# Performance work log

Measured on AMD Instinct MI355X. Metric: run time of the kernel, lower is better.

Reference implementation:

```python
import jax, jax.numpy as jnp
import numpy as np

EPS = 1e-5

def layer_norm(x, w, b):
    mu = x.mean(-1, keepdims=True)
    var = x.var(-1, keepdims=True)
    return (x - mu) / jnp.sqrt(var + EPS) * w + b

def moe_ffn(y, gW, W1, b1, W2, b2, topk):
    # y: [B,N,d]; W1: [E,d,f]; W2: [E,f,d].  Dense-equivalent of the
    # torch gather/compute/scatter-add dispatch: every expert runs on every
    # token, combined with top-k gate weights (zero for unselected experts).
    gate = jax.nn.softmax(y @ gW, axis=-1)                       # [B,N,E]
    w, sel = jax.lax.top_k(gate, topk)                           # [B,N,k]
    onehot = jax.nn.one_hot(sel, gW.shape[-1], dtype=y.dtype)    # [B,N,k,E]
    comb = jnp.einsum('bnk,bnke->bne', w, onehot)                # combine weights
    hmid = jax.nn.gelu(jnp.einsum('bnd,edf->bnef', y, W1) + b1, approximate=False)
    eo = jnp.einsum('bnef,efd->bned', hmid, W2) + b2             # [B,N,E,d]
    out = jnp.einsum('bne,bned->bnd', comb, eo)
    mask = onehot.sum(2)                                         # [B,N,E] 0/1
    cnt = mask.sum((0, 1))                                       # tokens per expert
    emb = jnp.einsum('bne,bnd->ed', mask, y) / jnp.maximum(cnt, 1.0)[:, None]
    return out, gate, emb

def setup_inputs():
    B, S, N = 8, 512, 1024
    d, H, E, f, L, topk = 512, 8, 8, 8, 2, 2   # d_ff == n_heads (repo quirk)
    key = jax.random.key(0)
    ks = iter(jax.random.split(key, 40))
    g = lambda shape, s=0.02: jax.random.normal(next(ks), shape, jnp.float32) * s
    return dict(
        x=jax.random.normal(next(ks), (B, S, N), jnp.float32),
        revin_w=jnp.ones((N,), jnp.float32) + g((N,), 0.01),
        revin_b=g((N,), 0.01),
        emb_W=g((S, d)), emb_b=g((d,)),
        Wq=g((L, d, d)), bq=g((L, d)),
        Wk=g((L, d, d)), bk=g((L, d)),
        Wv=g((L, d, d)), bv=g((L, d)),
        Wo=g((L, d, d)), bo=g((L, d)),
        ln1_w=jnp.ones((L, d), jnp.float32), ln1_b=jnp.zeros((L, d), jnp.float32),
        ln2_w=jnp.ones((L, d), jnp.float32), ln2_b=jnp.zeros((L, d), jnp.float32),
        gate_W=g((L, d, E)),
        eW1=g((L, E, d, f)), eb1=g((L, E, f)),
        eW2=g((L, E, f, d)), eb2=g((L, E, d)),
        enc_norm_w=jnp.ones((d,), jnp.float32), enc_norm_b=jnp.zeros((d,), jnp.float32),
        head_gate_W=g((d, E)),
        head_W=g((E, d, d)), head_b=g((E, d)),
        topk=topk, n_heads=H,
    )

def reference(x, revin_w, revin_b, emb_W, emb_b, Wq, bq, Wk, bk, Wv, bv, Wo, bo,
              ln1_w, ln1_b, ln2_w, ln2_b, gate_W, eW1, eb1, eW2, eb2,
              enc_norm_w, enc_norm_b, head_gate_W, head_W, head_b, topk, n_heads):
    B, S, N = x.shape
    d = emb_W.shape[1]
    H = n_heads
    dh = d // H
    L = Wq.shape[0]
    # RevIN normalize over time per variable (dropout layers are eval/identity)
    xv = jnp.swapaxes(x, 1, 2)                                   # [B,N,S]
    mean = xv.mean(-1, keepdims=True)
    std = jnp.sqrt(xv.var(-1, keepdims=True) + EPS)
    xn = (xv - mean) / std * revin_w[None, :, None] + revin_b[None, :, None]
    # DataEmbedding_inverted: Linear over the time axis -> variable tokens
    h = xn @ emb_W + emb_b                                       # [B,N,d]
    for l in range(L):
        q = (h @ Wq[l] + bq[l]).reshape(B, N, H, dh)
        k = (h @ Wk[l] + bk[l]).reshape(B, N, H, dh)
        v = (h @ Wv[l] + bv[l]).reshape(B, N, H, dh)
        attn = jax.nn.softmax(jnp.einsum('bnhe,bmhe->bhnm', q, k) / jnp.sqrt(jnp.float32(dh)), axis=-1)
        o = jnp.einsum('bhnm,bmhe->bnhe', attn, v).reshape(B, N, d) @ Wo[l] + bo[l]
        h = layer_norm(h + o, ln1_w[l], ln1_b[l])
        ffn, _gate, _emb = moe_ffn(h, gate_W[l], eW1[l], eb1[l], eW2[l], eb2[l], topk)
        h = layer_norm(h + ffn, ln2_w[l], ln2_b[l])
    h = layer_norm(h, enc_norm_w, enc_norm_b)
    # MoE projection head: experts are Linear(d, d)
    gate = jax.nn.softmax(h @ head_gate_W, axis=-1)
    w, sel = jax.lax.top_k(gate, topk)
    onehot = jax.nn.one_hot(sel, head_gate_W.shape[-1], dtype=h.dtype)
    comb = jnp.einsum('bnk,bnke->bne', w, onehot)
    eo = jnp.einsum('bnd,edf->bnef', h, head_W) + head_b         # [B,N,E,d]
    out = jnp.einsum('bne,bned->bnd', comb, eo)                  # [B,N,d]
    # RevIN denorm applied on [B, d_model, N]
    o2 = jnp.swapaxes(out, 1, 2)
    o2 = (o2 - revin_b[None, None, :]) / (revin_w[None, None, :] + 1e-10)
    o2 = o2 * jnp.swapaxes(std, 1, 2) + jnp.swapaxes(mean, 1, 2)
    return jnp.swapaxes(o2, 1, 2)                                # [B, n_vars, d_model]
```

## Files before the change

kernel.cpp:

```cpp
#include <hip/hip_runtime.h>
#include <math.h>

#define BATCH 8
#define SEQ 512
#define NVAR 1024
#define DM 512
#define NH 8
#define DH 64
#define NE 8
#define NF 8
#define NL 2
#define NTOK (BATCH*NVAR)
#define LN_EPS 1e-5f
#define LSC 2048.0f
#define ILSC (1.0f/2048.0f)

typedef __attribute__((ext_vector_type(8))) _Float16 f16x8;
typedef __attribute__((ext_vector_type(2))) _Float16 f16x2;
typedef __attribute__((ext_vector_type(4))) float f32x4;
#define MFMA16 __builtin_amdgcn_mfma_f32_16x16x32_f16

__device__ __forceinline__ void fsplit(float v, _Float16& hi, _Float16& lo) {
    hi = (_Float16)v;
    lo = (_Float16)((v - (float)hi) * LSC);
}
__device__ __forceinline__ float frec(_Float16 hi, _Float16 lo) {
    return (float)hi + (float)lo * ILSC;
}
__device__ __forceinline__ void fsplit2(float a, float b, f16x2& h2, f16x2& l2) {
    h2 = __builtin_bit_cast(f16x2, __builtin_amdgcn_cvt_pkrtz(a, b));
    l2 = __builtin_bit_cast(f16x2, __builtin_amdgcn_cvt_pkrtz(
             (a - (float)h2.x)*LSC, (b - (float)h2.y)*LSC));
}

__device__ __forceinline__ void gload_lds16(const _Float16* g, _Float16* l) {
    __builtin_amdgcn_global_load_lds(
        (const __attribute__((address_space(1))) void*)g,
        (__attribute__((address_space(3))) void*)l, 16, 0, 0);
}

#define DPPROR(v, C) __int_as_float(__builtin_amdgcn_update_dpp(0, __float_as_int(v), (C), 0xF, 0xF, true))
__device__ __forceinline__ float rowmax16(float v) {
    v = fmaxf(v, DPPROR(v, 0x121));
    v = fmaxf(v, DPPROR(v, 0x122));
    v = fmaxf(v, DPPROR(v, 0x124));
    v = fmaxf(v, DPPROR(v, 0x128));
    return v;
}
__device__ __forceinline__ float rowsum16(float v) {
    v += DPPROR(v, 0x121);
    v += DPPROR(v, 0x122);
    v += DPPROR(v, 0x124);
    v += DPPROR(v, 0x128);
    return v;
}

__global__ __launch_bounds__(256) void revin_stats_kernel(
        const float* __restrict__ x, float* __restrict__ mean, float* __restrict__ stdd) {
    int blk = blockIdx.x;
    int b = blk >> 4;
    int n0 = (blk & 15) << 6;
    int t = threadIdx.x;
    int ni = t & 63, sg = t >> 6;
    float s = 0.f, ss = 0.f;
    for (int sidx = sg; sidx < SEQ; sidx += 4) {
        float v = x[((size_t)b*SEQ + sidx)*NVAR + n0 + ni];
        s += v; ss += v*v;
    }
    __shared__ float rs[4][64], rq[4][64];
    rs[sg][ni] = s; rq[sg][ni] = ss;
    __syncthreads();
    if (t < 64) {
        float su = rs[0][t] + rs[1][t] + rs[2][t] + rs[3][t];
        float sq = rq[0][t] + rq[1][t] + rq[2][t] + rq[3][t];
        float m  = su / (float)SEQ;
        float var = sq / (float)SEQ - m*m;
        int n = n0 + t;
        mean[b*NVAR + n] = m;
        stdd[b*NVAR + n] = sqrtf(var + LN_EPS);
    }
}

__global__ __launch_bounds__(256) void revin_norm_kernel(
        const float* __restrict__ x, const float* __restrict__ mean, const float* __restrict__ stdd,
        const float* __restrict__ rw, const float* __restrict__ rb,
        _Float16* __restrict__ xnhi, _Float16* __restrict__ xnlo) {
    __shared__ float tile[32][33];
    int n0 = blockIdx.x << 5, s0 = blockIdx.y << 5, b = blockIdx.z;
    int t = threadIdx.x;
    int j = t & 31, i0 = t >> 5;
    for (int ii = i0; ii < 32; ii += 8)
        tile[ii][j] = x[((size_t)b*SEQ + s0 + ii)*NVAR + n0 + j];
    __syncthreads();
    int si = t & 31, j0 = t >> 5;
    for (int nj = j0; nj < 32; nj += 8) {
        int n = n0 + nj;
        float m = mean[b*NVAR + n], sd = stdd[b*NVAR + n];
        float v = (tile[si][nj] - m) / sd * rw[n] + rb[n];
        _Float16 h_, l_; fsplit(v, h_, l_);
        size_t idx = ((size_t)b*NVAR + n)*SEQ + s0 + si;
        xnhi[idx] = h_; xnlo[idx] = l_;
    }
}

struct WSrcs { const float* p[9]; };
__global__ __launch_bounds__(256) void transpose_w_kernel(
        WSrcs srcs, _Float16* __restrict__ whi, _Float16* __restrict__ wlo) {
    const float* W = srcs.p[blockIdx.z];
    _Float16* oh = whi + (size_t)blockIdx.z * DM * DM;
    _Float16* ol = wlo + (size_t)blockIdx.z * DM * DM;
    __shared__ float tile[64][65];
    int k0 = blockIdx.x << 6, n0 = blockIdx.y << 6;
    int t = threadIdx.x;
    for (int idx = t; idx < 4096; idx += 256) {
        int k = idx >> 6, n = idx & 63;
        tile[k][n] = W[(size_t)(k0 + k)*DM + n0 + n];
    }
    __syncthreads();
    for (int idx = t; idx < 4096; idx += 256) {
        int n = idx >> 6, k = idx & 63;
        _Float16 h_, l_; fsplit(tile[k][n], h_, l_);
        size_t o = (size_t)(n0 + n)*DM + k0 + k;
        oh[o] = h_; ol[o] = l_;
    }
}

__global__ __launch_bounds__(256) void gemm_f16x2_kernel(
        const _Float16* __restrict__ Ahg, const _Float16* __restrict__ Alg,
        const _Float16* __restrict__ Whg, const _Float16* __restrict__ Wlg,
        const float* __restrict__ bias, float* __restrict__ C,
        _Float16* __restrict__ Chi, _Float16* __restrict__ Clo,
        int M, int K, int N) {
    __shared__ _Float16 smem[24576];
    int id = blockIdx.x + (blockIdx.y << 3);
    int rm = ((id & 7) << 6) | (id >> 3);
    int bm = (rm >> 3) << 7, bn = (rm & 7) << 6;
    int t = threadIdx.x;
    int w = t >> 6, lane = t & 63, m16 = lane & 15, quad = lane >> 4;
    int wv = __builtin_amdgcn_readfirstlane(w);
    int lrow = lane >> 2, lcol = (lane & 3) << 3;
    f32x4 a1[2][4] = {}, a2[2][4] = {};

    #define G_STAGE(c, kk) do {                                              \
        _Pragma("unroll")                                                    \
        for (int ch = 0; ch < 2; ++ch) {                                     \
            size_t ga = (size_t)(bm + wv*32 + ch*16 + lrow)*K + (kk) + lcol; \
            gload_lds16(&Ahg[ga], &smem[(c)*4096 + (wv*32 + ch*16)*32]);     \
            gload_lds16(&Alg[ga], &smem[8192 + (c)*4096 + (wv*32 + ch*16)*32]); \
        }                                                                    \
        size_t gb = (size_t)(bn + wv*16 + lrow)*K + (kk) + lcol;             \
        gload_lds16(&Whg[gb], &smem[16384 + (c)*2048 + (wv*16)*32]);         \
        gload_lds16(&Wlg[gb], &smem[20480 + (c)*2048 + (wv*16)*32]);         \
    } while (0)

    G_STAGE(0, 0);
    int cur = 0;
    for (int k0 = 0; k0 < K; k0 += 32, cur ^= 1) {
        __syncthreads();
        if (k0 + 32 < K) G_STAGE(cur ^ 1, k0 + 32);
        const _Float16* AH = &smem[cur*4096];
        const _Float16* AL = &smem[8192 + cur*4096];
        const _Float16* BH = &smem[16384 + cur*2048];
        const _Float16* BL = &smem[20480 + cur*2048];
        f16x8 bh_[4], bl_[4];
#pragma unroll
        for (int nt = 0; nt < 4; ++nt) {
            bh_[nt] = *(const f16x8*)&BH[(nt*16 + m16)*32 + quad*8];
            bl_[nt] = *(const f16x8*)&BL[(nt*16 + m16)*32 + quad*8];
        }
#pragma unroll
        for (int h2 = 0; h2 < 2; ++h2) {
            f16x8 ah = *(const f16x8*)&AH[(w*32 + h2*16 + m16)*32 + quad*8];
            f16x8 al = *(const f16x8*)&AL[(w*32 + h2*16 + m16)*32 + quad*8];
#pragma unroll
            for (int nt = 0; nt < 4; ++nt) {
                a1[h2][nt] = MFMA16(ah, bh_[nt], a1[h2][nt], 0, 0, 0);
                a2[h2][nt] = MFMA16(ah, bl_[nt], a2[h2][nt], 0, 0, 0);
                a2[h2][nt] = MFMA16(al, bh_[nt], a2[h2][nt], 0, 0, 0);
            }
        }
    }
    #undef G_STAGE
#pragma unroll
    for (int h2 = 0; h2 < 2; ++h2)
#pragma unroll
        for (int nt = 0; nt < 4; ++nt) {
            int col = bn + nt*16 + m16;
            float bv = bias[col];
#pragma unroll
            for (int r = 0; r < 4; ++r) {
                size_t row = bm + w*32 + h2*16 + quad*4 + r;
                float v = a1[h2][nt][r] + a2[h2][nt][r]*ILSC + bv;
                if (C) C[row*N + col] = v;
                if (Chi) {
                    _Float16 h_, l_; fsplit(v, h_, l_);
                    Chi[row*N + col] = h_; Clo[row*N + col] = l_;
                }
            }
        }
}

__global__ __launch_bounds__(256) void gemm_qkvt_kernel(
        const _Float16* __restrict__ Ahg, const _Float16* __restrict__ Alg,
        const _Float16* __restrict__ Wqkh, const _Float16* __restrict__ Wqkl,
        const _Float16* __restrict__ Wvh,  const _Float16* __restrict__ Wvl,
        const float* __restrict__ biasQ, const float* __restrict__ biasK,
        const float* __restrict__ biasV,
        _Float16* __restrict__ Qhi, _Float16* __restrict__ Qlo,
        _Float16* __restrict__ KKhi, _Float16* __restrict__ KKlo,
        _Float16* __restrict__ vthi, _Float16* __restrict__ vtlo) {
    __shared__ _Float16 smem[24576];
    int t = threadIdx.x;
    int w = t >> 6, lane = t & 63, m16 = lane & 15, quad = lane >> 4;
    int wv = __builtin_amdgcn_readfirstlane(w);
    int lrow = lane >> 2, lcol = (lane & 3) << 3;

    if (blockIdx.x < 1024) {
        int id = blockIdx.x;
        int rm = ((id & 7) << 7) | (id >> 3);
        int bm = (rm >> 4) << 7, bn = (rm & 15) << 6;
        f32x4 a1[2][4] = {}, a2[2][4] = {};
        #define QK_STAGE(c, kk) do {                                             \
            _Pragma("unroll")                                                    \
            for (int ch = 0; ch < 2; ++ch) {                                     \
                size_t ga = (size_t)(bm + wv*32 + ch*16 + lrow)*DM + (kk) + lcol;\
                gload_lds16(&Ahg[ga], &smem[(c)*4096 + (wv*32 + ch*16)*32]);     \
                gload_lds16(&Alg[ga], &smem[8192 + (c)*4096 + (wv*32 + ch*16)*32]); \
            }                                                                    \
            size_t gb = (size_t)(bn + wv*16 + lrow)*DM + (kk) + lcol;            \
            gload_lds16(&Wqkh[gb], &smem[16384 + (c)*2048 + (wv*16)*32]);        \
            gload_lds16(&Wqkl[gb], &smem[20480 + (c)*2048 + (wv*16)*32]);        \
        } while (0)
        QK_STAGE(0, 0);
        int cur = 0;
        for (int k0 = 0; k0 < DM; k0 += 32, cur ^= 1) {
            __syncthreads();
            if (k0 + 32 < DM) QK_STAGE(cur ^ 1, k0 + 32);
            const _Float16* AH = &smem[cur*4096];
            const _Float16* AL = &smem[8192 + cur*4096];
            const _Float16* BH = &smem[16384 + cur*2048];
            const _Float16* BL = &smem[20480 + cur*2048];
            f16x8 bh_[4], bl_[4];
#pragma unroll
            for (int nt = 0; nt < 4; ++nt) {
                bh_[nt] = *(const f16x8*)&BH[(nt*16 + m16)*32 + quad*8];
                bl_[nt] = *(const f16x8*)&BL[(nt*16 + m16)*32 + quad*8];
            }
#pragma unroll
            for (int h2 = 0; h2 < 2; ++h2) {
                f16x8 ah = *(const f16x8*)&AH[(w*32 + h2*16 + m16)*32 + quad*8];
                f16x8 al = *(const f16x8*)&AL[(w*32 + h2*16 + m16)*32 + quad*8];
#pragma unroll
                for (int nt = 0; nt < 4; ++nt) {
                    a1[h2][nt] = MFMA16(ah, bh_[nt], a1[h2][nt], 0, 0, 0);
                    a2[h2][nt] = MFMA16(ah, bl_[nt], a2[h2][nt], 0, 0, 0);
                    a2[h2][nt] = MFMA16(al, bh_[nt], a2[h2][nt], 0, 0, 0);
                }
            }
        }
        #undef QK_STAGE
        const float* bias = (bn < 512) ? biasQ : biasK;
        _Float16* Ohi = (bn < 512) ? Qhi : KKhi;
        _Float16* Olo = (bn < 512) ? Qlo : KKlo;
        int cb = (bn < 512) ? bn : bn - 512;
#pragma unroll
        for (int h2 = 0; h2 < 2; ++h2)
#pragma unroll
            for (int nt = 0; nt < 4; ++nt) {
                int col = cb + nt*16 + m16;
                float bv = bias[col];
#pragma unroll
                for (int r = 0; r < 4; ++r) {
                    size_t row = bm + w*32 + h2*16 + quad*4 + r;
                    float v = a1[h2][nt][r] + a2[h2][nt][r]*ILSC + bv;
                    _Float16 h_, l_; fsplit(v, h_, l_);
                    Ohi[row*DM + col] = h_; Olo[row*DM + col] = l_;
                }
            }
        return;
    }
    {
        int id = blockIdx.x - 1024;
        int rm = ((id & 7) << 6) | (id >> 3);
        int bm = (rm >> 3) << 7, bn = (rm & 7) << 6;
        f32x4 a1[2][4] = {}, a2[2][4] = {};
        #define VT_STAGE(c, kk) do {                                             \
            _Pragma("unroll")                                                    \
            for (int ch = 0; ch < 2; ++ch) {                                     \
                size_t ga = (size_t)(bm + wv*32 + ch*16 + lrow)*DM + (kk) + lcol;\
                gload_lds16(&Ahg[ga], &smem[(c)*4096 + (wv*32 + ch*16)*32]);     \
                gload_lds16(&Alg[ga], &smem[8192 + (c)*4096 + (wv*32 + ch*16)*32]); \
            }                                                                    \
            size_t gb = (size_t)(bn + wv*16 + lrow)*DM + (kk) + lcol;            \
            gload_lds16(&Wvh[gb], &smem[16384 + (c)*2048 + (wv*16)*32]);         \
            gload_lds16(&Wvl[gb], &smem[20480 + (c)*2048 + (wv*16)*32]);         \
        } while (0)
        VT_STAGE(0, 0);
        int cur = 0;
        for (int k0 = 0; k0 < DM; k0 += 32, cur ^= 1) {
            __syncthreads();
            if (k0 + 32 < DM) VT_STAGE(cur ^ 1, k0 + 32);
            const _Float16* AH = &smem[cur*4096];
            const _Float16* AL = &smem[8192 + cur*4096];
            const _Float16* BH = &smem[16384 + cur*2048];
            const _Float16* BL = &smem[20480 + cur*2048];
            f16x8 bh_[4], bl_[4];
#pragma unroll
            for (int nt = 0; nt < 4; ++nt) {
                bh_[nt] = *(const f16x8*)&BH[(nt*16 + m16)*32 + quad*8];
                bl_[nt] = *(const f16x8*)&BL[(nt*16 + m16)*32 + quad*8];
            }
#pragma unroll
            for (int h2 = 0; h2 < 2; ++h2) {
                f16x8 ah = *(const f16x8*)&AH[(w*32 + h2*16 + m16)*32 + quad*8];
                f16x8 al = *(const f16x8*)&AL[(w*32 + h2*16 + m16)*32 + quad*8];
#pragma unroll
                for (int nt = 0; nt < 4; ++nt) {
                    a1[h2][nt] = MFMA16(ah, bh_[nt], a1[h2][nt], 0, 0, 0);
                    a2[h2][nt] = MFMA16(ah, bl_[nt], a2[h2][nt], 0, 0, 0);
                    a2[h2][nt] = MFMA16(al, bh_[nt], a2[h2][nt], 0, 0, 0);
                }
            }
        }
        #undef VT_STAGE
        __syncthreads();
        float (*Ct)[65] = (float (*)[65])smem;
#pragma unroll
        for (int h2 = 0; h2 < 2; ++h2)
#pragma unroll
            for (int nt = 0; nt < 4; ++nt) {
                float bv = biasV[bn + nt*16 + m16];
#pragma unroll
                for (int r = 0; r < 4; ++r)
                    Ct[w*32 + h2*16 + quad*4 + r][nt*16 + m16] = a1[h2][nt][r] + a2[h2][nt][r]*ILSC + bv;
            }
        __syncthreads();
        int b = bm >> 10, tokn0 = bm & 1023, hh = bn >> 6;
        int dh = t >> 2, tg = (t & 3) << 4;
        size_t rowb = ((size_t)(b*8 + hh)*64 + dh)*NVAR + tokn0;
        for (int hb = 0; hb < 2; ++hb) {
            int tl0 = hb*64 + tg;
            unsigned short hbuf[16], lbuf[16];
#pragma unroll
            for (int i = 0; i < 16; ++i) {
                _Float16 h_, l_; fsplit(Ct[tl0 + i][dh], h_, l_);
                hbuf[i] = __builtin_bit_cast(unsigned short, h_);
                lbuf[i] = __builtin_bit_cast(unsigned short, l_);
            }
            uint4 uh0, uh1, ul0, ul1;
            uh0.x = hbuf[0]|(hbuf[1]<<16);  uh0.y = hbuf[2]|(hbuf[3]<<16);
            uh0.z = hbuf[4]|(hbuf[5]<<16);  uh0.w = hbuf[6]|(hbuf[7]<<16);
            uh1.x = hbuf[8]|(hbuf[9]<<16);  uh1.y = hbuf[10]|(hbuf[11]<<16);
            uh1.z = hbuf[12]|(hbuf[13]<<16);uh1.w = hbuf[14]|(hbuf[15]<<16);
            ul0.x = lbuf[0]|(lbuf[1]<<16);  ul0.y = lbuf[2]|(lbuf[3]<<16);
            ul0.z = lbuf[4]|(lbuf[5]<<16);  ul0.w = lbuf[6]|(lbuf[7]<<16);
            ul1.x = lbuf[8]|(lbuf[9]<<16);  ul1.y = lbuf[10]|(lbuf[11]<<16);
            ul1.z = lbuf[12]|(lbuf[13]<<16);ul1.w = lbuf[14]|(lbuf[15]<<16);
            *(uint4*)&vthi[rowb + tl0]     = uh0;
            *(uint4*)&vthi[rowb + tl0 + 8] = uh1;
            *(uint4*)&vtlo[rowb + tl0]     = ul0;
            *(uint4*)&vtlo[rowb + tl0 + 8] = ul1;
        }
    }
}

__global__ __launch_bounds__(256, 4) void attn_f16x2_kernel(
        const _Float16* __restrict__ qh, const _Float16* __restrict__ ql,
        const _Float16* __restrict__ kh, const _Float16* __restrict__ kl,
        const _Float16* __restrict__ vth, const _Float16* __restrict__ vtl,
        _Float16* __restrict__ oh, _Float16* __restrict__ ol) {
    __shared__ _Float16 Kh[64][72], Kl[64][72];
    __shared__ _Float16 Vh[64][72], Vl[64][72];
    int blk = blockIdx.x;
    blk = ((blk & 7) << 7) | (blk >> 3);
    int qt = blk & 15, bh = blk >> 4;
    int b = bh >> 3, hh = bh & 7;
    int q0 = qt << 6;
    int t = threadIdx.x;
    int w = t >> 6, lane = t & 63;
    int m16 = lane & 15, quad = lane >> 4;
    size_t bbase = (size_t)b * NVAR;
    size_t vbase = (size_t)bh * DH * NVAR;

    f16x8 qfh[2], qfl[2];
#pragma unroll
    for (int ks = 0; ks < 2; ++ks) {
        size_t gq = (bbase + q0 + w*16 + m16)*DM + hh*DH + ks*32 + quad*8;
        qfh[ks] = *(const f16x8*)&qh[gq] * (_Float16)0.125f;
        qfl[ks] = *(const f16x8*)&ql[gq] * (_Float16)0.125f;
    }

    float mrow[4] = {-1e30f,-1e30f,-1e30f,-1e30f};
    float lrow[4] = {0.f,0.f,0.f,0.f};
    f32x4 o1[4] = {}, o2[4] = {};

    for (int n0 = 0; n0 < NVAR; n0 += 64) {
        for (int idx = t; idx < 512; idx += 256) {
            int r = idx >> 3, cg = (idx & 7) << 3;
            size_t gk = (bbase + n0 + r)*DM + hh*DH + cg;
            size_t gv = vbase + (size_t)r*NVAR + n0 + cg;
            *(uint4*)&Kh[r][cg] = *(const uint4*)&kh[gk];
            *(uint4*)&Kl[r][cg] = *(const uint4*)&kl[gk];
            *(uint4*)&Vh[r][cg] = *(const uint4*)&vth[gv];
            *(uint4*)&Vl[r][cg] = *(const uint4*)&vtl[gv];
        }
        __syncthreads();

        f32x4 s1[4] = {}, s2[4] = {};
#pragma unroll
        for (int ks = 0; ks < 2; ++ks) {
#pragma unroll
            for (int nt = 0; nt < 4; ++nt) {
                f16x8 bh_ = *(const f16x8*)&Kh[nt*16 + m16][ks*32 + quad*8];
                f16x8 bl_ = *(const f16x8*)&Kl[nt*16 + m16][ks*32 + quad*8];
                s1[nt] = MFMA16(qfh[ks], bh_, s1[nt], 0, 0, 0);
                s2[nt] = MFMA16(qfh[ks], bl_, s2[nt], 0, 0, 0);
                s2[nt] = MFMA16(qfl[ks], bh_, s2[nt], 0, 0, 0);
            }
        }
        __syncthreads();

        float pbuf[4][4];
        float mx[4];
#pragma unroll
        for (int r = 0; r < 4; ++r) {
            float sv0 = fmaf(s2[0][r], ILSC, s1[0][r]);
            float sv1 = fmaf(s2[1][r], ILSC, s1[1][r]);
            float sv2 = fmaf(s2[2][r], ILSC, s1[2][r]);
            float sv3 = fmaf(s2[3][r], ILSC, s1[3][r]);
            pbuf[0][r] = sv0; pbuf[1][r] = sv1; pbuf[2][r] = sv2; pbuf[3][r] = sv3;
            mx[r] = rowmax16(fmaxf(fmaxf(sv0, sv1), fmaxf(sv2, sv3)));
        }
        bool grow = (mx[0] > mrow[0]) | (mx[1] > mrow[1]) |
                    (mx[2] > mrow[2]) | (mx[3] > mrow[3]);
        if (__any(grow)) {
#pragma unroll
            for (int r = 0; r < 4; ++r) {
                float mnew = fmaxf(mrow[r], mx[r]);
                float alpha = __expf(mrow[r] - mnew);
                mrow[r] = mnew;
                lrow[r] *= alpha;
#pragma unroll
                for (int nt = 0; nt < 4; ++nt) { o1[nt][r] *= alpha; o2[nt][r] *= alpha; }
            }
        }
#pragma unroll
        for (int r = 0; r < 4; ++r) {
            float p0 = __expf(pbuf[0][r] - mrow[r]);
            float p1 = __expf(pbuf[1][r] - mrow[r]);
            float p2 = __expf(pbuf[2][r] - mrow[r]);
            float p3 = __expf(pbuf[3][r] - mrow[r]);
            lrow[r] += rowsum16(p0 + p1 + p2 + p3);
            pbuf[0][r] = p0; pbuf[1][r] = p1; pbuf[2][r] = p2; pbuf[3][r] = p3;
        }
#pragma unroll
        for (int nt = 0; nt < 4; ++nt)
#pragma unroll
            for (int rp = 0; rp < 2; ++rp) {
                f16x2 h2, l2;
                fsplit2(pbuf[nt][2*rp], pbuf[nt][2*rp + 1], h2, l2);
                Kh[w*16 + quad*4 + 2*rp][nt*16 + m16]     = h2.x;
                Kh[w*16 + quad*4 + 2*rp + 1][nt*16 + m16] = h2.y;
                Kl[w*16 + quad*4 + 2*rp][nt*16 + m16]     = l2.x;
                Kl[w*16 + quad*4 + 2*rp + 1][nt*16 + m16] = l2.y;
            }

#pragma unroll
        for (int ks = 0; ks < 2; ++ks) {
            f16x8 ph = *(const f16x8*)&Kh[w*16 + m16][ks*32 + quad*8];
            f16x8 pl = *(const f16x8*)&Kl[w*16 + m16][ks*32 + quad*8];
#pragma unroll
            for (int nt = 0; nt < 4; ++nt) {
                f16x8 vh_ = *(const f16x8*)&Vh[nt*16 + m16][ks*32 + quad*8];
                f16x8 vl_ = *(const f16x8*)&Vl[nt*16 + m16][ks*32 + quad*8];
                o1[nt] = MFMA16(ph, vh_, o1[nt], 0, 0, 0);
                o2[nt] = MFMA16(ph, vl_, o2[nt], 0, 0, 0);
                o2[nt] = MFMA16(pl, vh_, o2[nt], 0, 0, 0);
            }
        }
        __syncthreads();
    }
#pragma unroll
    for (int r = 0; r < 4; ++r) {
        float inv = 1.0f / lrow[r];
        size_t rowp = (bbase + q0 + w*16 + quad*4 + r)*DM + hh*DH;
        float ovv[4];
#pragma unroll
        for (int nt = 0; nt < 4; ++nt)
            ovv[nt] = fmaf(o2[nt][r], ILSC, o1[nt][r]) * inv;
#pragma unroll
        for (int np = 0; np < 2; ++np) {
            f16x2 h2, l2;
            fsplit2(ovv[2*np], ovv[2*np + 1], h2, l2);
            oh[rowp + (2*np)*16 + m16]     = h2.x;
            oh[rowp + (2*np + 1)*16 + m16] = h2.y;
            ol[rowp + (2*np)*16 + m16]     = l2.x;
            ol[rowp + (2*np + 1)*16 + m16] = l2.y;
        }
    }
}

__global__ __launch_bounds__(256) void ln_kernel(
        _Float16* __restrict__ hhi, _Float16* __restrict__ hlo,
        const float* __restrict__ res,
        const float* __restrict__ w, const float* __restrict__ b) {
    int rowi = blockIdx.x, t = threadIdx.x;
    size_t base = (size_t)rowi * DM;
    int c = t << 1;
    f16x2 hv = *(const f16x2*)&hhi[base + c];
    f16x2 lv = *(const f16x2*)&hlo[base + c];
    float v0 = frec(hv.x, lv.x);
    float v1 = frec(hv.y, lv.y);
    if (res) { float2 rv = *(const float2*)&res[base + c]; v0 += rv.x; v1 += rv.y; }
    float s = v0 + v1, q = v0*v0 + v1*v1;
#pragma unroll
    for (int off = 1; off < 64; off <<= 1) {
        s += __shfl_xor(s, off);
        q += __shfl_xor(q, off);
    }
    __shared__ float sred[4], qred[4];
    int wid = t >> 6, lane = t & 63;
    if (lane == 0) { sred[wid] = s; qred[wid] = q; }
    __syncthreads();
    s = sred[0] + sred[1] + sred[2] + sred[3];
    q = qred[0] + qred[1] + qred[2] + qred[3];
    float m = s / (float)DM;
    float var = q / (float)DM - m*m;
    float inv = 1.0f / sqrtf(var + LN_EPS);
    float2 wv = *(const float2*)&w[c];
    float2 bv = *(const float2*)&b[c];
    float y0 = (v0 - m)*inv * wv.x + bv.x;
    float y1 = (v1 - m)*inv * wv.y + bv.y;
    f16x2 h2, l2; fsplit2(y0, y1, h2, l2);
    *(f16x2*)&hhi[base + c] = h2;
    *(f16x2*)&hlo[base + c] = l2;
}

__device__ __forceinline__ float gelu_exact(float xv) {
    return 0.5f * xv * (1.0f + erff(xv * 0.70710678118654752f));
}

__global__ __launch_bounds__(256) void moe_ln_kernel(
        _Float16* __restrict__ hhi, _Float16* __restrict__ hlo,
        const float* __restrict__ gW, const float* __restrict__ W1, const float* __restrict__ b1,
        const float* __restrict__ W2, const float* __restrict__ b2,
        const float* __restrict__ lw, const float* __restrict__ lb) {
    int tok = blockIdx.x, t = threadIdx.x;
    __shared__ float hs[DM];
    __shared__ float red[32][8];
    __shared__ float glog[8];
    __shared__ float hmid[8];
    __shared__ float wsel[2];
    __shared__ int   esel[2];
    __shared__ float sred[4], qred[4];
    size_t base = (size_t)tok * DM;
    int c = t << 1;
    f16x2 hv = *(const f16x2*)&hhi[base + c];
    f16x2 lv = *(const f16x2*)&hlo[base + c];
    float hv0 = frec(hv.x, lv.x);
    float hv1 = frec(hv.y, lv.y);
    hs[c] = hv0; hs[c + 1] = hv1;
    __syncthreads();
    int e = t & 7, i0 = t >> 3;
    {
        float a = 0.f;
        for (int i = i0; i < DM; i += 32) a += hs[i] * gW[i*NE + e];
        red[i0][e] = a;
    }
    __syncthreads();
    if (t < 8) { float sv = 0.f; for (int i = 0; i < 32; ++i) sv += red[i][t]; glog[t] = sv; }
    __syncthreads();
    if (t == 0) {
        float m0 = -1e30f, m1 = -1e30f; int s0i = 0, s1i = 0;
        for (int ei = 0; ei < 8; ++ei) {
            float vv = glog[ei];
            if (vv > m0) { m1 = m0; s1i = s0i; m0 = vv; s0i = ei; }
            else if (vv > m1) { m1 = vv; s1i = ei; }
        }
        float Z = 0.f;
        for (int ei = 0; ei < 8; ++ei) Z += expf(glog[ei] - m0);
        wsel[0] = 1.0f / Z;
        wsel[1] = expf(m1 - m0) / Z;
        esel[0] = s0i; esel[1] = s1i;
    }
    __syncthreads();
    float o0 = 0.f, o1 = 0.f;
    for (int ks = 0; ks < 2; ++ks) {
        int ee = esel[ks]; float wk = wsel[ks];
        int f = t & 7;
        float a = 0.f;
        for (int i = i0; i < DM; i += 32) a += hs[i] * W1[((size_t)ee*DM + i)*NF + f];
        red[i0][f] = a;
        __syncthreads();
        if (t < 8) {
            float sv = b1[ee*NF + t];
            for (int i = 0; i < 32; ++i) sv += red[i][t];
            hmid[t] = gelu_exact(sv);
        }
        __syncthreads();
        float2 b2v = *(const float2*)&b2[ee*DM + c];
        float s0v = b2v.x, s1v = b2v.y;
#pragma unroll
        for (int i = 0; i < NF; ++i) {
            float hm = hmid[i];
            float2 wpv = *(const float2*)&W2[((size_t)ee*NF + i)*DM + c];
            s0v += hm * wpv.x; s1v += hm * wpv.y;
        }
        o0 += wk * s0v; o1 += wk * s1v;
        __syncthreads();
    }
    float v0 = hv0 + o0, v1 = hv1 + o1;
    float s = v0 + v1, q = v0*v0 + v1*v1;
#pragma unroll
    for (int off = 1; off < 64; off <<= 1) {
        s += __shfl_xor(s, off);
        q += __shfl_xor(q, off);
    }
    int wid = t >> 6, lane = t & 63;
    if (lane == 0) { sred[wid] = s; qred[wid] = q; }
    __syncthreads();
    s = sred[0] + sred[1] + sred[2] + sred[3];
    q = qred[0] + qred[1] + qred[2] + qred[3];
    float m = s / (float)DM;
    float var = q / (float)DM - m*m;
    float inv = 1.0f / sqrtf(var + LN_EPS);
    float2 wv = *(const float2*)&lw[c];
    float2 bv = *(const float2*)&lb[c];
    float y0 = (v0 - m)*inv * wv.x + bv.x;
    float y1 = (v1 - m)*inv * wv.y + bv.y;
    f16x2 h2o, l2o; fsplit2(y0, y1, h2o, l2o);
    *(f16x2*)&hhi[base + c] = h2o;
    *(f16x2*)&hlo[base + c] = l2o;
}

__global__ __launch_bounds__(256) void encln_gate_kernel(
        _Float16* __restrict__ hhi, _Float16* __restrict__ hlo,
        const float* __restrict__ lw, const float* __restrict__ lb,
        const float* __restrict__ gW,
        int* __restrict__ sel, float2* __restrict__ wpair,
        int* __restrict__ cnt) {
    int tok = blockIdx.x, t = threadIdx.x;
    if (tok == 0 && t < NE) cnt[t] = 0;
    __shared__ float hs[DM];
    __shared__ float red[32][8];
    __shared__ float glog[8];
    __shared__ float sred[4], qred[4];
    size_t base = (size_t)tok * DM;
    int c = t << 1;
    f16x2 hv = *(const f16x2*)&hhi[base + c];
    f16x2 lv = *(const f16x2*)&hlo[base + c];
    float v0 = frec(hv.x, lv.x);
    float v1 = frec(hv.y, lv.y);
    float s = v0 + v1, q = v0*v0 + v1*v1;
#pragma unroll
    for (int off = 1; off < 64; off <<= 1) {
        s += __shfl_xor(s, off);
        q += __shfl_xor(q, off);
    }
    int wid = t >> 6, lane = t & 63;
    if (lane == 0) { sred[wid] = s; qred[wid] = q; }
    __syncthreads();
    s = sred[0] + sred[1] + sred[2] + sred[3];
    q = qred[0] + qred[1] + qred[2] + qred[3];
    float m = s / (float)DM;
    float var = q / (float)DM - m*m;
    float inv = 1.0f / sqrtf(var + LN_EPS);
    float2 wv = *(const float2*)&lw[c];
    float2 bv = *(const float2*)&lb[c];
    float y0 = (v0 - m)*inv * wv.x + bv.x;
    float y1 = (v1 - m)*inv * wv.y + bv.y;
    f16x2 h2o, l2o; fsplit2(y0, y1, h2o, l2o);
    *(f16x2*)&hhi[base + c] = h2o;
    *(f16x2*)&hlo[base + c] = l2o;
    hs[c] = y0; hs[c + 1] = y1;
    __syncthreads();
    int e = t & 7, i0 = t >> 3;
    float a = 0.f;
    for (int i = i0; i < DM; i += 32) a += hs[i] * gW[i*NE + e];
    red[i0][e] = a;
    __syncthreads();
    if (t < 8) { float sv = 0.f; for (int i = 0; i < 32; ++i) sv += red[i][t]; glog[t] = sv; }
    __syncthreads();
    if (t == 0) {
        float m0 = -1e30f, m1 = -1e30f; int s0i = 0, s1i = 0;
        for (int ei = 0; ei < 8; ++ei) {
            float vv = glog[ei];
            if (vv > m0) { m1 = m0; s1i = s0i; m0 = vv; s0i = ei; }
            else if (vv > m1) { m1 = vv; s1i = ei; }
        }
        float Z = 0.f;
        for (int ei = 0; ei < 8; ++ei) Z += __expf(glog[ei] - m0);
        float2 wvv;
        wvv.x = 1.0f / Z;
        wvv.y = __expf(m1 - m0) / Z;
        sel[tok] = s0i | (s1i << 3);
        wpair[tok] = wvv;
    }
}

__global__ __launch_bounds__(64) void head_bucket_kernel(
        const int* __restrict__ sel, const float2* __restrict__ wpair,
        int* __restrict__ cnt, int* __restrict__ idxlist, float* __restrict__ wlist,
        int* __restrict__ pos0, int* __restrict__ pos1) {
    int lane = threadIdx.x;
    int tok = blockIdx.x*64 + lane;
    int s = sel[tok];
    int s0 = s & 7, s1 = (s >> 3) & 7;
    float2 wv = wpair[tok];
    unsigned long long lmask = (lane == 63) ? 0x7FFFFFFFFFFFFFFFull
                                            : ((1ull << lane) - 1ull);
#pragma unroll
    for (int e = 0; e < NE; ++e) {
        unsigned long long m0 = __ballot(s0 == e);
        unsigned long long m1 = __ballot(s1 == e);
        int tot = __popcll(m0) + __popcll(m1);
        int basep = 0;
        if (lane == 0 && tot > 0) basep = atomicAdd(&cnt[e], tot);
        basep = __shfl(basep, 0);
        if (s0 == e) {
            int p = basep + __popcll(m0 & lmask);
            idxlist[e*NTOK + p] = tok; wlist[e*NTOK + p] = wv.x;
            pos0[tok] = (e << 16) | p;
        }
        if (s1 == e) {
            int p = basep + __popcll(m0) + __popcll(m1 & lmask);
            idxlist[e*NTOK + p] = tok; wlist[e*NTOK + p] = wv.y;
            pos1[tok] = (e << 16) | p;
        }
    }
}

__global__ __launch_bounds__(64) void head_prefix_kernel(int* __restrict__ cnt) {
    if (threadIdx.x == 0) {
        int run = 0, trun = 0;
        for (int e = 0; e < NE; ++e) {
            cnt[8 + e]  = run;  run  += cnt[e];
            cnt[16 + e] = trun; trun += (cnt[e] + 63) >> 6;
        }
        cnt[24] = trun;
    }
}

__global__ __launch_bounds__(256) void head_gemm_f16x2_kernel(
        const _Float16* __restrict__ hhi, const _Float16* __restrict__ hlo,
        const _Float16* __restrict__ hwhi, const _Float16* __restrict__ hwlo,
        const float* __restrict__ Hb,
        const int* __restrict__ cnt, const int* __restrict__ idxlist,
        const float* __restrict__ wlist, float* __restrict__ slotf) {
    int item = blockIdx.x;
    int total = cnt[24];
    if (item >= 2*total) return;
    int bn   = (item & 1) << 8;
    int tile = item >> 1;
    int e = 0;
#pragma unroll
    for (int ei = 1; ei < NE; ++ei) if (tile >= cnt[16 + ei]) e = ei;
    int m0 = (tile - cnt[16 + e]) << 6;
    int cnt_e = cnt[e];
    int rv = cnt_e - m0; if (rv > 64) rv = 64;
    int pref_e = cnt[8 + e];
    int t = threadIdx.x;
    int w = t >> 6, lane = t & 63, m16 = lane & 15, quad = lane >> 4;

    __shared__ _Float16 sAh[64][40], sAl[64][40];
    __shared__ _Float16 sBh[256][40], sBl[256][40];
    __shared__ int   idxs[64];
    __shared__ float ws[64];
    if (t < 64) {
        if (t < rv) { idxs[t] = idxlist[e*NTOK + m0 + t]; ws[t] = wlist[e*NTOK + m0 + t]; }
        else        { idxs[t] = idxlist[e*NTOK + m0];     ws[t] = 0.f; }
    }
    __syncthreads();

    const _Float16* Wh = hwhi + (size_t)e*DM*DM;
    const _Float16* Wl = hwlo + (size_t)e*DM*DM;
    int ra = t >> 2, ca = (t & 3) << 3;
    f32x4 a1[4][4] = {}, a2[4][4] = {};
    for (int k0 = 0; k0 < DM; k0 += 32) {
        size_t ga = (size_t)idxs[ra]*DM + k0 + ca;
        *(uint4*)&sAh[ra][ca] = *(const uint4*)&hhi[ga];
        *(uint4*)&sAl[ra][ca] = *(const uint4*)&hlo[ga];
#pragma unroll
        for (int p = 0; p < 4; ++p) {
            int rb = p*64 + ra;
            size_t gb = (size_t)(bn + rb)*DM + k0 + ca;
            *(uint4*)&sBh[rb][ca] = *(const uint4*)&Wh[gb];
            *(uint4*)&sBl[rb][ca] = *(const uint4*)&Wl[gb];
        }
        __syncthreads();
        f16x8 ah[4], al[4];
#pragma unroll
        for (int mt = 0; mt < 4; ++mt) {
            ah[mt] = *(const f16x8*)&sAh[mt*16 + m16][quad*8];
            al[mt] = *(const f16x8*)&sAl[mt*16 + m16][quad*8];
        }
#pragma unroll
        for (int nt = 0; nt < 4; ++nt) {
            f16x8 bh_ = *(const f16x8*)&sBh[w*64 + nt*16 + m16][quad*8];
            f16x8 bl_ = *(const f16x8*)&sBl[w*64 + nt*16 + m16][quad*8];
#pragma unroll
            for (int mt = 0; mt < 4; ++mt) {
                a1[mt][nt] = MFMA16(ah[mt], bh_, a1[mt][nt], 0, 0, 0);
                a2[mt][nt] = MFMA16(ah[mt], bl_, a2[mt][nt], 0, 0, 0);
                a2[mt][nt] = MFMA16(al[mt], bh_, a2[mt][nt], 0, 0, 0);
            }
        }
        __syncthreads();
    }
#pragma unroll
    for (int mt = 0; mt < 4; ++mt)
#pragma unroll
        for (int r = 0; r < 4; ++r) {
            int rloc = mt*16 + quad*4 + r;
            if (rloc < rv) {
                float wk = ws[rloc];
                size_t srow = (size_t)(pref_e + m0 + rloc)*DM;
#pragma unroll
                for (int nt = 0; nt < 4; ++nt) {
                    int gcol = bn + w*64 + nt*16 + m16;
                    float v = a1[mt][nt][r] + a2[mt][nt][r]*ILSC + Hb[e*DM + gcol];
                    slotf[srow + gcol] = wk * v;
                }
            }
        }
}

__global__ __launch_bounds__(256) void head_combine_kernel(
        const float* __restrict__ slotf,
        const int* __restrict__ pos0, const int* __restrict__ pos1,
        const int* __restrict__ cnt,
        const float* __restrict__ rw, const float* __restrict__ rb,
        const float* __restrict__ mean, const float* __restrict__ stdd,
        float* __restrict__ out) {
    int tok = blockIdx.x, t = threadIdx.x;
    int n = tok & (NVAR - 1);
    int e0enc = pos0[tok], e1enc = pos1[tok];
    size_t s0 = (size_t)(cnt[8 + (e0enc >> 16)] + (e0enc & 0xFFFF)) * DM;
    size_t s1 = (size_t)(cnt[8 + (e1enc >> 16)] + (e1enc & 0xFFFF)) * DM;
    size_t base = (size_t)tok * DM;
    float mn = mean[tok], sd = stdd[tok];
    float rwv = rw[n] + 1e-10f, rbv = rb[n];
    float o0 = slotf[s0 + t] + slotf[s1 + t];
    float o1 = slotf[s0 + t + 256] + slotf[s1 + t + 256];
    out[base + t]       = (o0 - rbv) / rwv * sd + mn;
    out[base + t + 256] = (o1 - rbv) / rwv * sd + mn;
}

extern "C" void kernel_launch(void* const* d_in, const int* in_sizes, int n_in,
                              void* d_out, int out_size, void* d_ws, size_t ws_size,
                              hipStream_t stream) {
    const float* x       = (const float*)d_in[0];
    const float* revin_w = (const float*)d_in[1];
    const float* revin_b = (const float*)d_in[2];
    const float* emb_W   = (const float*)d_in[3];
    const float* emb_b   = (const float*)d_in[4];
    const float* Wq      = (const float*)d_in[5];
    const float* bq      = (const float*)d_in[6];
    const float* Wk      = (const float*)d_in[7];
    const float* bk      = (const float*)d_in[8];
    const float* Wv      = (const float*)d_in[9];
    const float* bv      = (const float*)d_in[10];
    const float* Wo      = (const float*)d_in[11];
    const float* bo      = (const float*)d_in[12];
    const float* ln1_w   = (const float*)d_in[13];
    const float* ln1_b   = (const float*)d_in[14];
    const float* ln2_w   = (const float*)d_in[15];
    const float* ln2_b   = (const float*)d_in[16];
    const float* gate_W  = (const float*)d_in[17];
    const float* eW1     = (const float*)d_in[18];
    const float* eb1     = (const float*)d_in[19];
    const float* eW2     = (const float*)d_in[20];
    const float* eb2     = (const float*)d_in[21];
    const float* enc_w   = (const float*)d_in[22];
    const float* enc_b   = (const float*)d_in[23];
    const float* hgW     = (const float*)d_in[24];
    const float* hW      = (const float*)d_in[25];
    const float* hb      = (const float*)d_in[26];
    float* out = (float*)d_out;

    const size_t TOKD = (size_t)NTOK * DM;
    float* ws   = (float*)d_ws;
    float* mean = ws;
    float* stdd = ws + 8192;
    _Float16* hhi  = (_Float16*)(ws + 16384);
    _Float16* hlo  = hhi + TOKD;
    _Float16* qhi  = hlo + TOKD;
    _Float16* qlo  = qhi + TOKD;
    _Float16* khi  = qlo + TOKD;
    _Float16* klo  = khi + TOKD;
    _Float16* vthi = klo + TOKD;
    _Float16* vtlo = vthi + TOKD;
    _Float16* whi  = vtlo + TOKD;
    _Float16* wlo  = whi + (size_t)9*DM*DM;
    int*   cnt     = (int*)(wlo + (size_t)9*DM*DM);
    int*   idxlist = cnt + 32;
    float* wlist   = (float*)(idxlist + NE*NTOK);
    int*   sel     = (int*)(wlist + NE*NTOK);
    float2* wpair  = (float2*)(sel + NTOK);
    int*   pos0    = (int*)(wpair + NTOK);
    int*   pos1    = pos0 + NTOK;
    float* proj    = (float*)khi;
    float* slotf   = (float*)qhi;

    dim3 blk(256);
    dim3 ggemm(DM/64, NTOK/128);

    revin_stats_kernel<<<dim3(BATCH*16), blk, 0, stream>>>(x, mean, stdd);
    revin_norm_kernel<<<dim3(NVAR/32, SEQ/32, BATCH), blk, 0, stream>>>(
        x, mean, stdd, revin_w, revin_b, qhi, qlo);

    WSrcs srcs;
    srcs.p[0] = emb_W;
    for (int l = 0; l < NL; ++l) {
        srcs.p[1 + l*4 + 0] = Wq + (size_t)l*DM*DM;
        srcs.p[1 + l*4 + 1] = Wk + (size_t)l*DM*DM;
        srcs.p[1 + l*4 + 2] = Wv + (size_t)l*DM*DM;
        srcs.p[1 + l*4 + 3] = Wo + (size_t)l*DM*DM;
    }
    transpose_w_kernel<<<dim3(8, 8, 9), blk, 0, stream>>>(srcs, whi, wlo);

    gemm_f16x2_kernel<<<ggemm, blk, 0, stream>>>(
        qhi, qlo, whi, wlo, emb_b, nullptr, hhi, hlo, NTOK, SEQ, DM);

    for (int l = 0; l < NL; ++l) {
        size_t oq = (size_t)(1 + l*4 + 0)*DM*DM;
        size_t ov = (size_t)(1 + l*4 + 2)*DM*DM;
        size_t oo = (size_t)(1 + l*4 + 3)*DM*DM;
        gemm_qkvt_kernel<<<dim3(1536), blk, 0, stream>>>(
            hhi, hlo, whi + oq, wlo + oq, whi + ov, wlo + ov,
            bq + l*DM, bk + l*DM, bv + l*DM,
            qhi, qlo, khi, klo, vthi, vtlo);
        attn_f16x2_kernel<<<dim3(64*16), blk, 0, stream>>>(
            qhi, qlo, khi, klo, vthi, vtlo, qhi, qlo);
        gemm_f16x2_kernel<<<ggemm, blk, 0, stream>>>(
            qhi, qlo, whi + oo, wlo + oo, bo + l*DM, proj, nullptr, nullptr, NTOK, DM, DM);
        ln_kernel<<<dim3(NTOK), blk, 0, stream>>>(hhi, hlo, proj, ln1_w + l*DM, ln1_b + l*DM);
        moe_ln_kernel<<<dim3(NTOK), blk, 0, stream>>>(
            hhi, hlo, gate_W + (size_t)l*DM*NE,
            eW1 + (size_t)l*NE*DM*NF, eb1 + (size_t)l*NE*NF,
            eW2 + (size_t)l*NE*NF*DM, eb2 + (size_t)l*NE*DM,
            ln2_w + l*DM, ln2_b + l*DM);
    }

    WSrcs hsrcs;
    for (int e = 0; e < NE; ++e) hsrcs.p[e] = hW + (size_t)e*DM*DM;
    hsrcs.p[8] = hW;
    transpose_w_kernel<<<dim3(8, 8, 8), blk, 0, stream>>>(hsrcs, vthi, vtlo);

    encln_gate_kernel<<<dim3(NTOK), blk, 0, stream>>>(
        hhi, hlo, enc_w, enc_b, hgW, sel, wpair, cnt);
    head_bucket_kernel<<<dim3(NTOK/64), dim3(64), 0, stream>>>(
        sel, wpair, cnt, idxlist, wlist, pos0, pos1);
    head_prefix_kernel<<<dim3(1), dim3(64), 0, stream>>>(cnt);
    head_gemm_f16x2_kernel<<<dim3(576), blk, 0, stream>>>(
        hhi, hlo, vthi, vtlo, hb, cnt, idxlist, wlist, slotf);
    head_combine_kernel<<<dim3(NTOK), blk, 0, stream>>>(
        slotf, pos0, pos1, cnt, revin_w, revin_b, mean, stdd, out);
}
```

Measured before the change: 813.5 us.

## Narrow head GEMM N-tile, use direct global-to-LDS loads, store slots as f16 pairs

The MoE head GEMM drops from a 64x256 to a 64x128 output tile per block, so the grid grows from 576 to 1088 blocks and accumulator registers shrink, which should improve occupancy. Tile staging now uses gload_lds16 direct global-to-LDS loads in a flat shared buffer instead of going through registers. The per-slot output is written as split f16 hi/lo halves instead of fp32, and the combine kernel reconstructs it with frec. This trades more blocks and reloading A per N-tile for better parallelism and less register pressure, with slightly lower slot precision.

```diff
diff --git a/kernel.cpp b/kernel.cpp
--- a/kernel.cpp
+++ b/kernel.cpp
@@ -746,12 +746,13 @@
         const _Float16* __restrict__ hwhi, const _Float16* __restrict__ hwlo,
         const float* __restrict__ Hb,
         const int* __restrict__ cnt, const int* __restrict__ idxlist,
-        const float* __restrict__ wlist, float* __restrict__ slotf) {
+        const float* __restrict__ wlist,
+        _Float16* __restrict__ slot_hi, _Float16* __restrict__ slot_lo) {
     int item = blockIdx.x;
     int total = cnt[24];
-    if (item >= 2*total) return;
-    int bn   = (item & 1) << 8;
-    int tile = item >> 1;
+    if (item >= 4*total) return;
+    int bn   = (item & 3) << 7;
+    int tile = item >> 2;
     int e = 0;
 #pragma unroll
     for (int ei = 1; ei < NE; ++ei) if (tile >= cnt[16 + ei]) e = ei;
@@ -761,43 +762,44 @@
     int pref_e = cnt[8 + e];
     int t = threadIdx.x;
     int w = t >> 6, lane = t & 63, m16 = lane & 15, quad = lane >> 4;
-
-    __shared__ _Float16 sAh[64][40], sAl[64][40];
-    __shared__ _Float16 sBh[256][40], sBl[256][40];
+    int wv = __builtin_amdgcn_readfirstlane(w);
+
+    __shared__ _Float16 smem[12288];
     __shared__ int   idxs[64];
     __shared__ float ws[64];
     if (t < 64) {
-        if (t < rv) { idxs[t] = idxlist[e*NTOK + m0 + t]; ws[t] = wlist[e*NTOK + m0 + t]; }
-        else        { idxs[t] = idxlist[e*NTOK + m0];     ws[t] = 0.f; }
-    }
-    __syncthreads();
+        int src = (t < rv) ? t : (rv - 1);
+        idxs[t] = idxlist[e*NTOK + m0 + src];
+        ws[t]   = (t < rv) ? wlist[e*NTOK + m0 + t] : 0.f;
+    }
+    __syncthreads();
+    int arow_tok = idxs[wv*16 + (lane >> 2)];
+    int lcol = (lane & 3) << 3;
 
     const _Float16* Wh = hwhi + (size_t)e*DM*DM;
     const _Float16* Wl = hwlo + (size_t)e*DM*DM;
-    int ra = t >> 2, ca = (t & 3) << 3;
-    f32x4 a1[4][4] = {}, a2[4][4] = {};
+    f32x4 a1[4][2] = {}, a2[4][2] = {};
     for (int k0 = 0; k0 < DM; k0 += 32) {
-        size_t ga = (size_t)idxs[ra]*DM + k0 + ca;
-        *(uint4*)&sAh[ra][ca] = *(const uint4*)&hhi[ga];
-        *(uint4*)&sAl[ra][ca] = *(const uint4*)&hlo[ga];
-#pragma unroll
-        for (int p = 0; p < 4; ++p) {
-            int rb = p*64 + ra;
-            size_t gb = (size_t)(bn + rb)*DM + k0 + ca;
-            *(uint4*)&sBh[rb][ca] = *(const uint4*)&Wh[gb];
-            *(uint4*)&sBl[rb][ca] = *(const uint4*)&Wl[gb];
+        size_t ga = (size_t)arow_tok*DM + k0 + lcol;
+        gload_lds16(&hhi[ga], &smem[(wv*16)*32]);
+        gload_lds16(&hlo[ga], &smem[2048 + (wv*16)*32]);
+#pragma unroll
+        for (int p = 0; p < 2; ++p) {
+            size_t gb = (size_t)(bn + wv*32 + p*16 + (lane >> 2))*DM + k0 + lcol;
+            gload_lds16(&Wh[gb], &smem[4096 + (wv*32 + p*16)*32]);
+            gload_lds16(&Wl[gb], &smem[8192 + (wv*32 + p*16)*32]);
         }
         __syncthreads();
         f16x8 ah[4], al[4];
 #pragma unroll
         for (int mt = 0; mt < 4; ++mt) {
-            ah[mt] = *(const f16x8*)&sAh[mt*16 + m16][quad*8];
-            al[mt] = *(const f16x8*)&sAl[mt*16 + m16][quad*8];
-        }
-#pragma unroll
-        for (int nt = 0; nt < 4; ++nt) {
-            f16x8 bh_ = *(const f16x8*)&sBh[w*64 + nt*16 + m16][quad*8];
-            f16x8 bl_ = *(const f16x8*)&sBl[w*64 + nt*16 + m16][quad*8];
+            ah[mt] = *(const f16x8*)&smem[(mt*16 + m16)*32 + quad*8];
+            al[mt] = *(const f16x8*)&smem[2048 + (mt*16 + m16)*32 + quad*8];
+        }
+#pragma unroll
+        for (int nt = 0; nt < 2; ++nt) {
+            f16x8 bh_ = *(const f16x8*)&smem[4096 + (w*32 + nt*16 + m16)*32 + quad*8];
+            f16x8 bl_ = *(const f16x8*)&smem[8192 + (w*32 + nt*16 + m16)*32 + quad*8];
 #pragma unroll
             for (int mt = 0; mt < 4; ++mt) {
                 a1[mt][nt] = MFMA16(ah[mt], bh_, a1[mt][nt], 0, 0, 0);
@@ -816,17 +818,19 @@
                 float wk = ws[rloc];
                 size_t srow = (size_t)(pref_e + m0 + rloc)*DM;
 #pragma unroll
-                for (int nt = 0; nt < 4; ++nt) {
-                    int gcol = bn + w*64 + nt*16 + m16;
-                    float v = a1[mt][nt][r] + a2[mt][nt][r]*ILSC + Hb[e*DM + gcol];
-                    slotf[srow + gcol] = wk * v;
+                for (int nt = 0; nt < 2; ++nt) {
+                    int gcol = bn + w*32 + nt*16 + m16;
+                    float v = wk * (a1[mt][nt][r] + a2[mt][nt][r]*ILSC + Hb[e*DM + gcol]);
+                    _Float16 h_, l_; fsplit(v, h_, l_);
+                    slot_hi[srow + gcol] = h_;
+                    slot_lo[srow + gcol] = l_;
                 }
             }
         }
 }
 
 __global__ __launch_bounds__(256) void head_combine_kernel(
-        const float* __restrict__ slotf,
+        const _Float16* __restrict__ slot_hi, const _Float16* __restrict__ slot_lo,
         const int* __restrict__ pos0, const int* __restrict__ pos1,
         const int* __restrict__ cnt,
         const float* __restrict__ rw, const float* __restrict__ rb,
@@ -840,8 +844,10 @@
     size_t base = (size_t)tok * DM;
     float mn = mean[tok], sd = stdd[tok];
     float rwv = rw[n] + 1e-10f, rbv = rb[n];
-    float o0 = slotf[s0 + t] + slotf[s1 + t];
-    float o1 = slotf[s0 + t + 256] + slotf[s1 + t + 256];
+    float o0 = frec(slot_hi[s0 + t], slot_lo[s0 + t])
+             + frec(slot_hi[s1 + t], slot_lo[s1 + t]);
+    float o1 = frec(slot_hi[s0 + t + 256], slot_lo[s0 + t + 256])
+             + frec(slot_hi[s1 + t + 256], slot_lo[s1 + t + 256]);
     out[base + t]       = (o0 - rbv) / rwv * sd + mn;
     out[base + t + 256] = (o1 - rbv) / rwv * sd + mn;
 }
@@ -900,7 +906,8 @@
     int*   pos0    = (int*)(wpair + NTOK);
     int*   pos1    = pos0 + NTOK;
     float* proj    = (float*)khi;
-    float* slotf   = (float*)qhi;
+    _Float16* slot_hi = qhi;
+    _Float16* slot_lo = khi;
 
     dim3 blk(256);
     dim3 ggemm(DM/64, NTOK/128);
@@ -952,8 +959,8 @@
     head_bucket_kernel<<<dim3(NTOK/64), dim3(64), 0, stream>>>(
         sel, wpair, cnt, idxlist, wlist, pos0, pos1);
     head_prefix_kernel<<<dim3(1), dim3(64), 0, stream>>>(cnt);
-    head_gemm_f16x2_kernel<<<dim3(576), blk, 0, stream>>>(
-        hhi, hlo, vthi, vtlo, hb, cnt, idxlist, wlist, slotf);
+    head_gemm_f16x2_kernel<<<dim3(1088), blk, 0, stream>>>(
+        hhi, hlo, vthi, vtlo, hb, cnt, idxlist, wlist, slot_hi, slot_lo);
     head_combine_kernel<<<dim3(NTOK), blk, 0, stream>>>(
-        slotf, pos0, pos1, cnt, revin_w, revin_b, mean, stdd, out);
-}
+        slot_hi, slot_lo, pos0, pos1, cnt, revin_w, revin_b, mean, stdd, out);
+}
```

Measured after the change: 770.7 us (median of 2 runs). -5.3%, faster.
